# Optimization experiments

Hardware: AMD Instinct MI355X
Metric: run time of the kernel (lower is better)

Reference implementation:

```python
import jax, jax.numpy as jnp
import numpy as np

N = 4096      # nodes
E = 131072    # edges (before self loops)
C = 512       # channels
H = 8         # heads
CO = C // H   # per-head out channels (64)
EPS = 1e-5
NEG_SLOPE = 0.2


def layer_norm(x, g, b):
    mu = jnp.mean(x, axis=-1, keepdims=True)
    var = jnp.mean((x - mu) ** 2, axis=-1, keepdims=True)
    return (x - mu) * jax.lax.rsqrt(var + EPS) * g + b


def gatv2(x, src, dst, wl, bl, wr, br, att, bias):
    # PyG GATv2Conv, concat=True, add_self_loops handled by caller.
    n = x.shape[0]
    xl = (x @ wl.T + bl).reshape(n, H, CO)   # target-side features
    xr = (x @ wr.T + br).reshape(n, H, CO)   # source-side features (messages)
    e = jax.nn.leaky_relu(xl[dst] + xr[src], NEG_SLOPE)   # [E+N, H, CO]
    alpha = jnp.einsum('ehc,hc->eh', e, att)              # [E+N, H]
    # segment softmax over destination neighborhoods
    amax = jax.ops.segment_max(alpha, dst, num_segments=n)
    ex = jnp.exp(alpha - amax[dst])
    denom = jax.ops.segment_sum(ex, dst, num_segments=n)
    a = ex / denom[dst]                                   # [E+N, H]
    msg = xr[src] * a[:, :, None]                         # [E+N, H, CO]
    out = jax.ops.segment_sum(msg, dst, num_segments=n)   # [N, H, CO]
    return out.reshape(n, H * CO) + bias


def mha(x, in_w, in_b, out_w, out_b):
    # nn.MultiheadAttention self-attention, batch=1, eval mode
    n = x.shape[0]
    qkv = x @ in_w.T + in_b                               # [N, 3C]
    q, k, v = jnp.split(qkv, 3, axis=-1)
    q = q.reshape(n, H, CO); k = k.reshape(n, H, CO); v = v.reshape(n, H, CO)
    scores = jnp.einsum('qhd,khd->hqk', q, k) / jnp.sqrt(jnp.float32(CO))
    p = jax.nn.softmax(scores, axis=-1)
    o = jnp.einsum('hqk,khd->qhd', p, v).reshape(n, C)
    return o @ out_w.T + out_b


def setup_inputs() -> dict:
    key = jax.random.key(0)
    ks = jax.random.split(key, 24)
    s = 0.02
    d = {}
    d['x'] = jax.random.normal(ks[0], (N, C), jnp.float32)
    d['edge_index'] = jax.random.randint(ks[1], (2, E), 0, N, dtype=jnp.int64)
    d['gat_wl'] = jax.random.normal(ks[2], (H * CO, C), jnp.float32) * s
    d['gat_bl'] = jnp.zeros((H * CO,), jnp.float32)
    d['gat_wr'] = jax.random.normal(ks[3], (H * CO, C), jnp.float32) * s
    d['gat_br'] = jnp.zeros((H * CO,), jnp.float32)
    d['gat_att'] = jax.random.normal(ks[4], (H, CO), jnp.float32) * s
    d['gat_b'] = jnp.zeros((H * CO,), jnp.float32)
    d['in_w'] = jax.random.normal(ks[5], (3 * C, C), jnp.float32) * s
    d['in_b'] = jnp.zeros((3 * C,), jnp.float32)
    d['out_w'] = jax.random.normal(ks[6], (C, C), jnp.float32) * s
    d['out_b'] = jnp.zeros((C,), jnp.float32)
    d['ln1_g'] = jnp.ones((C,), jnp.float32); d['ln1_b'] = jnp.zeros((C,), jnp.float32)
    d['ln2_g'] = jnp.ones((C,), jnp.float32); d['ln2_b'] = jnp.zeros((C,), jnp.float32)
    d['ln3_g'] = jnp.ones((C,), jnp.float32); d['ln3_b'] = jnp.zeros((C,), jnp.float32)
    d['w1'] = jax.random.normal(ks[7], (4 * C, C), jnp.float32) * s
    d['b1'] = jnp.zeros((4 * C,), jnp.float32)
    d['w2'] = jax.random.normal(ks[8], (C, 4 * C), jnp.float32) * s
    d['b2'] = jnp.zeros((C,), jnp.float32)
    return d


def reference(x, edge_index, gat_wl, gat_bl, gat_wr, gat_br, gat_att, gat_b,
              in_w, in_b, out_w, out_b, ln1_g, ln1_b, ln2_g, ln2_b,
              ln3_g, ln3_b, w1, b1, w2, b2):
    n = x.shape[0]
    loops = jnp.arange(n, dtype=edge_index.dtype)
    src = jnp.concatenate([edge_index[0], loops])
    dst = jnp.concatenate([edge_index[1], loops])
    h_local = gatv2(x, src, dst, gat_wl, gat_bl, gat_wr, gat_br, gat_att, gat_b)
    x = layer_norm(x + h_local, ln1_g, ln1_b)
    h_global = mha(x, in_w, in_b, out_w, out_b)
    x = layer_norm(x + h_global, ln2_g, ln2_b)
    h_ffn = (jax.nn.gelu(x @ w1.T + b1, approximate=False)) @ w2.T + b2
    x = layer_norm(x + h_ffn, ln3_g, ln3_b)
    return x
```

## Files before the change

kernel.cpp:

```cpp
#include <hip/hip_runtime.h>
#include <math.h>

#define NN 4096
#define CC 512
#define EE 131072
#define NEDGE (EE + NN)
#define HH 8
#define DCO 64
#define NC2 2097152L

typedef __attribute__((ext_vector_type(8))) short bfrag;
typedef __attribute__((ext_vector_type(4))) float f32x4;
typedef __attribute__((ext_vector_type(4))) int i32x4;

__device__ __forceinline__ float bf2f(unsigned short u) {
  union { float f; unsigned int i; } x; x.i = ((unsigned int)u) << 16; return x.f;
}
__device__ __forceinline__ unsigned short f2bf(float f) {
  union { float f; unsigned int i; } x; x.f = f;
  unsigned int r = x.i + 0x7FFFu + ((x.i >> 16) & 1u);
  return (unsigned short)(r >> 16);
}
__device__ __forceinline__ unsigned short f2bf_trunc(float f) {
  union { float f; unsigned int i; } x; x.f = f;
  return (unsigned short)(x.i >> 16);
}

__device__ __forceinline__ void gld16(const unsigned short* g, unsigned short* l) {
  __builtin_amdgcn_global_load_lds(
      (__attribute__((address_space(1))) unsigned int*)g,
      (__attribute__((address_space(3))) unsigned int*)l, 16, 0, 0);
}

#define QSC 0.18033688011112042f

#define CX  2097152L
#define CWL (CX + 262144L)
#define CWR (CWL + 262144L)
#define CIW (CWR + 786432L)
#define COW (CIW + 262144L)
#define CW1 (COW + 1048576L)
#define CW2 (CW1 + 1048576L)

__global__ void cvt_all(const float* __restrict__ x, const float* __restrict__ wl,
                        const float* __restrict__ wr, const float* __restrict__ iw,
                        const float* __restrict__ ow, const float* __restrict__ w1,
                        const float* __restrict__ w2, unsigned short* __restrict__ dst,
                        int* __restrict__ cntcur, const float* __restrict__ bl,
                        const float* __restrict__ br, float* __restrict__ biasc) {
  if (blockIdx.x >= 5632) {
    int t = threadIdx.x;
    if (blockIdx.x == 5632) {
      for (int k = t; k < 8192; k += 256) cntcur[k] = 0;
    } else {
      for (int k = t; k < 512; k += 256) {
        biasc[k] = bl[k];
        biasc[512 + k] = br[k];
      }
    }
    return;
  }
  long i = ((long)blockIdx.x * 256 + threadIdx.x) * 4;
  const float* s; long o;
  if (i < CX)       { s = x;  o = i; }
  else if (i < CWL) { s = wl; o = i - CX; }
  else if (i < CWR) { s = wr; o = i - CWL; }
  else if (i < CIW) { s = iw; o = i - CWR; }
  else if (i < COW) { s = ow; o = i - CIW; }
  else if (i < CW1) { s = w1; o = i - COW; }
  else              { s = w2; o = i - CW1; }
  f32x4 v = *(const f32x4*)(s + o);
  union { unsigned long long q; unsigned short u[4]; } t;
#pragma unroll
  for (int j = 0; j < 4; j++) t.u[j] = f2bf(v[j]);
  *(unsigned long long*)(dst + i) = t.q;
}

template<int OMODE, int TN, bool SPLIT>
__global__ __launch_bounds__(256) void gemm_t(
    const unsigned short* __restrict__ A, const unsigned short* __restrict__ B,
    const float* __restrict__ bias, void* __restrict__ C,
    int K, int lda, int ldb, int ldc)
{
  __shared__ unsigned short As[4096];
  __shared__ unsigned short Bs[TN * 32];
  constexpr int MI = (TN == 128) ? 4 : 2;
  const int tid = threadIdx.x;
  const int wave = tid >> 6, lane = tid & 63;
  const int ml = lane & 15, kq = lane >> 4;
  const int wm = (TN == 128) ? ((wave >> 1) << 6) : (wave << 5);
  const int wn = (TN == 128) ? ((wave & 1) << 6) : 0;
  const int bm = blockIdx.y << 7, bn = blockIdx.x * TN;
  const int srow = tid >> 2, scol = (tid & 3) << 3;
  if (SPLIT) { A += (long)blockIdx.z * K; B += (long)blockIdx.z * K; }
  const float* biasp = (!SPLIT || blockIdx.z == 0) ? bias : nullptr;
  const unsigned short* Ag = A + (long)(bm + srow) * lda + scol;
  const unsigned short* Bg = B + (long)(bn + srow) * ldb + scol;
  const long astep = (long)64 * lda, bstep = (long)64 * ldb;
  unsigned short* lA0 = As + tid * 8;
  unsigned short* lA1 = As + 2048 + tid * 8;
  unsigned short* lB0 = Bs + tid * 8;
  f32x4 acc[MI][4];
#pragma unroll
  for (int mi = 0; mi < MI; mi++)
#pragma unroll
    for (int ni = 0; ni < 4; ni++) acc[mi][ni] = (f32x4){0.f, 0.f, 0.f, 0.f};
  for (int k0 = 0; k0 < K; k0 += 32) {
    __syncthreads();
    gld16(Ag, lA0); gld16(Ag + astep, lA1);
    gld16(Bg, lB0);
    if (TN == 128) gld16(Bg + bstep, Bs + 2048 + tid * 8);
    Ag += 32; Bg += 32;
    __syncthreads();
    bfrag af[MI], bf[4];
#pragma unroll
    for (int mi = 0; mi < MI; mi++)
      af[mi] = *(const bfrag*)&As[(wm + (mi << 4) + ml) * 32 + (kq << 3)];
#pragma unroll
    for (int ni = 0; ni < 4; ni++)
      bf[ni] = *(const bfrag*)&Bs[(wn + (ni << 4) + ml) * 32 + (kq << 3)];
#pragma unroll
    for (int mi = 0; mi < MI; mi++)
#pragma unroll
      for (int ni = 0; ni < 4; ni++)
        acc[mi][ni] = __builtin_amdgcn_mfma_f32_16x16x32_bf16(af[mi], bf[ni], acc[mi][ni], 0, 0, 0);
  }
#pragma unroll
  for (int ni = 0; ni < 4; ni++) {
    int col = bn + wn + (ni << 4) + ml;
    float bb = biasp ? biasp[col] : 0.f;
#pragma unroll
    for (int mi = 0; mi < MI; mi++) {
      int row0 = bm + wm + (mi << 4) + (kq << 2);
#pragma unroll
      for (int r = 0; r < 4; r++) {
        float v = acc[mi][ni][r] + bb;
        int row = row0 + r;
        if (OMODE == 3) {
          unsigned short* q = (unsigned short*)C;
          if (col < 512) {
            int h = col >> 6, d = col & 63;
            q[(long)h * (NN * DCO) + (long)row * DCO + d] = f2bf(v * QSC);
          } else if (col < 1024) {
            int c2 = col - 512, h = c2 >> 6, d = c2 & 63;
            q[NC2 + (long)h * (NN * DCO) + (long)row * DCO + d] = f2bf(v);
          } else {
            int c2 = col - 1024, h = c2 >> 6, d = c2 & 63;
            q[2 * NC2 + (long)h * (DCO * NN) + (long)d * NN + row] = f2bf(v);
          }
        } else if (OMODE == 0) {
          long off = (SPLIT ? (long)blockIdx.z * NC2 : 0) + (long)row * ldc + col;
          ((float*)C)[off] = v;
        } else {
          if (OMODE == 2) v = 0.5f * v * (1.f + erff(v * 0.70710678118f));
          ((unsigned short*)C)[(long)row * ldc + col] = f2bf(v);
        }
      }
    }
  }
}

__global__ void count_k(const int* __restrict__ ei, int* __restrict__ cnt) {
  int e = blockIdx.x * 256 + threadIdx.x;
  if (e >= NEDGE) return;
  int d = (e < EE) ? ei[EE + e] : (e - EE);
  atomicAdd(&cnt[d], 1);
}

__global__ void scan_k(const int* __restrict__ cnt, int* __restrict__ rowptr) {
  __shared__ int s[1024];
  int t = threadIdx.x;
  int b = t * 4;
  int c0 = cnt[b], c1 = cnt[b + 1], c2 = cnt[b + 2], c3 = cnt[b + 3];
  int sum = c0 + c1 + c2 + c3;
  s[t] = sum;
  __syncthreads();
  for (int o = 1; o < 1024; o <<= 1) {
    int v = (t >= o) ? s[t - o] : 0;
    __syncthreads();
    s[t] += v;
    __syncthreads();
  }
  int ex = s[t] - sum;
  rowptr[b] = ex; rowptr[b + 1] = ex + c0;
  rowptr[b + 2] = ex + c0 + c1; rowptr[b + 3] = ex + c0 + c1 + c2;
  if (t == 1023) rowptr[4096] = ex + sum;
}

__global__ void scatter_k(const int* __restrict__ ei, const int* __restrict__ rowptr,
                          int* __restrict__ cur, int* __restrict__ order) {
  int e = blockIdx.x * 256 + threadIdx.x;
  if (e >= NEDGE) return;
  int d = (e < EE) ? ei[EE + e] : (e - EE);
  int p = atomicAdd(&cur[d], 1);
  order[rowptr[d] + p] = e;
}

__global__ __launch_bounds__(256) void gat_fused(
    const unsigned short* __restrict__ xlr, const float* __restrict__ x,
    const int* __restrict__ order, const int* __restrict__ rowptr,
    const int* __restrict__ ei, const float* __restrict__ att,
    const float* __restrict__ gbias,
    const float* __restrict__ g, const float* __restrict__ be,
    float* __restrict__ of, unsigned short* __restrict__ ob)
{
  __shared__ float part[4][512];
  __shared__ float sw[4][8];
  __shared__ float sinv[8];
  __shared__ float shl[8];
  int n = blockIdx.x, t = threadIdx.x;
  int beg = rowptr[n], deg = rowptr[n + 1] - beg;
  int wave = t >> 6, lane = t & 63;
  int ch = lane << 3;
  union U8 { i32x4 v; unsigned short u[8]; };
  U8 XL; XL.v = *(const i32x4*)(xlr + (long)n * 1024 + ch);
  float xl[8];
#pragma unroll
  for (int j = 0; j < 8; j++) xl[j] = bf2f(XL.u[j]);
  f32x4 t0 = *(const f32x4*)(att + ch);
  f32x4 t1 = *(const f32x4*)(att + ch + 4);
  float acc[8];
#pragma unroll
  for (int j = 0; j < 8; j++) acc[j] = 0.f;
  float se = 0.f;
  int i = wave;
  U8 X;
  if (i < deg) {
    int e = order[beg + i];
    int sn = (e < EE) ? ei[e] : (e - EE);
    X.v = *(const i32x4*)(xlr + (long)sn * 1024 + 512 + ch);
  }
  while (i < deg) {
    U8 Xc = X;
    int inext = i + 4;
    if (inext < deg) {
      int e = order[beg + inext];
      int sn = (e < EE) ? ei[e] : (e - EE);
      X.v = *(const i32x4*)(xlr + (long)sn * 1024 + 512 + ch);
    }
    float xr[8];
    float p = 0.f;
#pragma unroll
    for (int j = 0; j < 8; j++) {
      xr[j] = bf2f(Xc.u[j]);
      float v = xl[j] + xr[j];
      v = (v > 0.f) ? v : 0.2f * v;
      float tv = (j < 4) ? t0[j] : t1[j - 4];
      p += tv * v;
    }
    p += __shfl_xor(p, 1); p += __shfl_xor(p, 2); p += __shfl_xor(p, 4);
    float ew = __expf(p);
    se += ew;
#pragma unroll
    for (int j = 0; j < 8; j++) acc[j] += ew * xr[j];
    i = inext;
  }
  *(f32x4*)&part[wave][ch]     = (f32x4){acc[0], acc[1], acc[2], acc[3]};
  *(f32x4*)&part[wave][ch + 4] = (f32x4){acc[4], acc[5], acc[6], acc[7]};
  if ((lane & 7) == 0) sw[wave][lane >> 3] = se;
  __syncthreads();
  if (t < 8) sinv[t] = 1.f / (sw[0][t] + sw[1][t] + sw[2][t] + sw[3][t]);
  __syncthreads();
  long base = (long)n * CC;
  float v0, v1;
  {
    int c = t;
    float p4 = part[0][c] + part[1][c] + part[2][c] + part[3][c];
    v0 = x[base + c] + p4 * sinv[c >> 6] + gbias[c];
  }
  {
    int c = t + 256;
    float p4 = part[0][c] + part[1][c] + part[2][c] + part[3][c];
    v1 = x[base + c] + p4 * sinv[c >> 6] + gbias[c];
  }
  float s = v0 + v1, ss = v0 * v0 + v1 * v1;
  for (int o = 32; o > 0; o >>= 1) { s += __shfl_down(s, o); ss += __shfl_down(ss, o); }
  if (lane == 0) { shl[wave] = s; shl[4 + wave] = ss; }
  __syncthreads();
  float S = shl[0] + shl[1] + shl[2] + shl[3];
  float SS = shl[4] + shl[5] + shl[6] + shl[7];
  float mean = S * (1.f / 512.f);
  float var = SS * (1.f / 512.f) - mean * mean;
  float rs = rsqrtf(var + 1e-5f);
  float y0 = (v0 - mean) * rs * g[t] + be[t];
  float y1 = (v1 - mean) * rs * g[t + 256] + be[t + 256];
  of[base + t] = y0; of[base + t + 256] = y1;
  ob[base + t] = f2bf(y0); ob[base + t + 256] = f2bf(y1);
}

template<int NS>
__global__ __launch_bounds__(256) void resid_ln(
    const float* __restrict__ a, const float* __restrict__ b,
    const float* __restrict__ g, const float* __restrict__ be,
    float* __restrict__ of, unsigned short* __restrict__ ob)
{
  __shared__ float sh[8];
  int row = blockIdx.x, t = threadIdx.x;
  long base = (long)row * CC;
  float b0 = 0.f, b1 = 0.f;
#pragma unroll
  for (int s = 0; s < NS; s++) {
    b0 += b[(long)s * NC2 + base + t];
    b1 += b[(long)s * NC2 + base + t + 256];
  }
  float v0 = a[base + t] + b0;
  float v1 = a[base + t + 256] + b1;
  float s = v0 + v1, ss = v0 * v0 + v1 * v1;
  for (int o = 32; o > 0; o >>= 1) { s += __shfl_down(s, o); ss += __shfl_down(ss, o); }
  int wave = t >> 6, lane = t & 63;
  if (lane == 0) { sh[wave] = s; sh[4 + wave] = ss; }
  __syncthreads();
  float S = sh[0] + sh[1] + sh[2] + sh[3];
  float SS = sh[4] + sh[5] + sh[6] + sh[7];
  float mean = S * (1.f / 512.f);
  float var = SS * (1.f / 512.f) - mean * mean;
  float rs = rsqrtf(var + 1e-5f);
  float y0 = (v0 - mean) * rs * g[t] + be[t];
  float y1 = (v1 - mean) * rs * g[t + 256] + be[t + 256];
  if (of) { of[base + t] = y0; of[base + t + 256] = y1; }
  if (ob) { ob[base + t] = f2bf(y0); ob[base + t + 256] = f2bf(y1); }
}

__global__ __launch_bounds__(256, 4) void flash_attn(
    const unsigned short* __restrict__ qkvP, unsigned short* __restrict__ Op,
    float* __restrict__ Lp)
{
  __shared__ unsigned short QP[128 * 72];
  __shared__ unsigned short Ks[64 * 72];
  __shared__ unsigned short Vs[64 * 72];
  const int tid = threadIdx.x;
  const int wave = tid >> 6, lane = tid & 63;
  const int ml = lane & 15, kq = lane >> 4;
  const int h = blockIdx.x & 7, qt = blockIdx.x >> 3;
  const int sp = blockIdx.y;
  const int n0 = qt << 7;
  const unsigned short* Qh = qkvP + (long)h * (NN * DCO);
  const unsigned short* Kh = qkvP + NC2 + (long)h * (NN * DCO);
  const unsigned short* Vh = qkvP + 2 * NC2 + (long)h * (DCO * NN);
  {
    int r = tid >> 1, c = (tid & 1) << 5;
    const unsigned short* src = Qh + (long)(n0 + r) * DCO + c;
    unsigned short* d = &QP[r * 72 + c];
    *(i32x4*)d        = *(const i32x4*)src;
    *(i32x4*)(d + 8)  = *(const i32x4*)(src + 8);
    *(i32x4*)(d + 16) = *(const i32x4*)(src + 16);
    *(i32x4*)(d + 24) = *(const i32x4*)(src + 24);
  }
  __syncthreads();
  bfrag aq[2][2];
#pragma unroll
  for (int s = 0; s < 2; s++)
#pragma unroll
    for (int kh = 0; kh < 2; kh++)
      aq[s][kh] = *(const bfrag*)&QP[(wave * 32 + s * 16 + ml) * 72 + kh * 32 + (kq << 3)];
  bfrag ones;
#pragma unroll
  for (int j = 0; j < 8; j++) ones[j] = (short)0x3F80;
  f32x4 Oa[2][4];
  f32x4 Lc[2];
#pragma unroll
  for (int s = 0; s < 2; s++) {
    Lc[s] = (f32x4){0.f, 0.f, 0.f, 0.f};
#pragma unroll
    for (int dg = 0; dg < 4; dg++) Oa[s][dg] = (f32x4){0.f, 0.f, 0.f, 0.f};
  }
  const int r_ = tid >> 2, c_ = (tid & 3) << 4;
  const int j0 = sp << 4;
  i32x4 ka, kb, va, vb;
  {
    int k0 = j0 << 6;
    ka = *(const i32x4*)(Kh + (long)(k0 + r_) * DCO + c_);
    kb = *(const i32x4*)(Kh + (long)(k0 + r_) * DCO + c_ + 8);
    va = *(const i32x4*)(Vh + (long)r_ * NN + k0 + c_);
    vb = *(const i32x4*)(Vh + (long)r_ * NN + k0 + c_ + 8);
  }
  for (int jj = 0; jj < 16; jj++) {
    if (jj) __syncthreads();
    *(i32x4*)&Ks[r_ * 72 + c_] = ka; *(i32x4*)&Ks[r_ * 72 + c_ + 8] = kb;
    *(i32x4*)&Vs[r_ * 72 + c_] = va; *(i32x4*)&Vs[r_ * 72 + c_ + 8] = vb;
    __syncthreads();
    if (jj < 15) {
      int k0 = (j0 + jj + 1) << 6;
      ka = *(const i32x4*)(Kh + (long)(k0 + r_) * DCO + c_);
      kb = *(const i32x4*)(Kh + (long)(k0 + r_) * DCO + c_ + 8);
      va = *(const i32x4*)(Vh + (long)r_ * NN + k0 + c_);
      vb = *(const i32x4*)(Vh + (long)r_ * NN + k0 + c_ + 8);
    }
    f32x4 sc[2][4];
#pragma unroll
    for (int s = 0; s < 2; s++)
#pragma unroll
      for (int c = 0; c < 4; c++) sc[s][c] = (f32x4){0.f, 0.f, 0.f, 0.f};
    __builtin_amdgcn_s_setprio(1);
#pragma unroll
    for (int c = 0; c < 4; c++) {
      bfrag bk0 = *(const bfrag*)&Ks[(c * 16 + ml) * 72 + (kq << 3)];
      bfrag bk1 = *(const bfrag*)&Ks[(c * 16 + ml) * 72 + 32 + (kq << 3)];
#pragma unroll
      for (int s = 0; s < 2; s++) {
        sc[s][c] = __builtin_amdgcn_mfma_f32_16x16x32_bf16(bk0, aq[s][0], sc[s][c], 0, 0, 0);
        sc[s][c] = __builtin_amdgcn_mfma_f32_16x16x32_bf16(bk1, aq[s][1], sc[s][c], 0, 0, 0);
      }
    }
    __builtin_amdgcn_s_setprio(0);
#pragma unroll
    for (int s = 0; s < 2; s++) {
#pragma unroll
      for (int c = 0; c < 4; c++) {
        unsigned int w0, w1;
        float e0, e1, e2, e3;
        asm("v_exp_f32 %2, %6\n\t"
            "v_exp_f32 %3, %7\n\t"
            "v_exp_f32 %4, %8\n\t"
            "v_exp_f32 %5, %9\n\t"
            "v_cvt_pk_bf16_f32 %0, %2, %3\n\t"
            "v_cvt_pk_bf16_f32 %1, %4, %5"
            : "=v"(w0), "=v"(w1), "=&v"(e0), "=&v"(e1), "=&v"(e2), "=&v"(e3)
            : "v"(sc[s][c][0]), "v"(sc[s][c][1]), "v"(sc[s][c][2]), "v"(sc[s][c][3]));
        union { unsigned long long q; unsigned int w[2]; } u;
        u.w[0] = w0; u.w[1] = w1;
        *(unsigned long long*)&QP[(wave * 32 + s * 16 + ml) * 72 + c * 16 + (kq << 2)] = u.q;
      }
    }
    bfrag ap[2][2];
#pragma unroll
    for (int s = 0; s < 2; s++)
#pragma unroll
      for (int kh = 0; kh < 2; kh++)
        ap[s][kh] = *(const bfrag*)&QP[(wave * 32 + s * 16 + ml) * 72 + kh * 32 + (kq << 3)];
    __builtin_amdgcn_s_setprio(1);
#pragma unroll
    for (int s = 0; s < 2; s++) {
      Lc[s] = __builtin_amdgcn_mfma_f32_16x16x32_bf16(ap[s][0], ones, Lc[s], 0, 0, 0);
      Lc[s] = __builtin_amdgcn_mfma_f32_16x16x32_bf16(ap[s][1], ones, Lc[s], 0, 0, 0);
    }
#pragma unroll
    for (int dg = 0; dg < 4; dg++) {
      bfrag bv0 = *(const bfrag*)&Vs[(dg * 16 + ml) * 72 + (kq << 3)];
      bfrag bv1 = *(const bfrag*)&Vs[(dg * 16 + ml) * 72 + 32 + (kq << 3)];
#pragma unroll
      for (int s = 0; s < 2; s++) {
        Oa[s][dg] = __builtin_amdgcn_mfma_f32_16x16x32_bf16(ap[s][0], bv0, Oa[s][dg], 0, 0, 0);
        Oa[s][dg] = __builtin_amdgcn_mfma_f32_16x16x32_bf16(ap[s][1], bv1, Oa[s][dg], 0, 0, 0);
      }
    }
    __builtin_amdgcn_s_setprio(0);
  }
  long obase = (long)sp * NC2;
#pragma unroll
  for (int s = 0; s < 2; s++)
#pragma unroll
    for (int dg = 0; dg < 4; dg++)
#pragma unroll
      for (int r = 0; r < 4; r++) {
        int row = wave * 32 + s * 16 + (kq << 2) + r;
        Op[obase + (long)(n0 + row) * CC + (h << 6) + (dg << 4) + ml] = f2bf(Oa[s][dg][r]);
      }
  if (ml == 0) {
#pragma unroll
    for (int s = 0; s < 2; s++)
#pragma unroll
      for (int r = 0; r < 4; r++) {
        int row = wave * 32 + s * 16 + (kq << 2) + r;
        Lp[(long)sp * (NN * HH) + (long)(n0 + row) * HH + h] = Lc[s][r];
      }
  }
}

__global__ void flash_combine(const unsigned short* __restrict__ Op,
                              const float* __restrict__ Lp,
                              unsigned short* __restrict__ Ao) {
  int idx = blockIdx.x * 256 + threadIdx.x;
  int n = idx >> 9, c = idx & 511, h = c >> 6;
  float l = 0.f, o = 0.f;
#pragma unroll
  for (int s = 0; s < 4; s++) {
    l += Lp[(long)s * (NN * HH) + (long)n * HH + h];
    o += bf2f(Op[(long)s * NC2 + idx]);
  }
  Ao[idx] = f2bf(o / l);
}

extern "C" void kernel_launch(void* const* d_in, const int* in_sizes, int n_in,
                              void* d_out, int out_size, void* d_ws, size_t ws_size,
                              hipStream_t stream) {
  typedef unsigned short u16;
  const float* x      = (const float*)d_in[0];
  const int*   ei     = (const int*)d_in[1];
  const float* wl     = (const float*)d_in[2];
  const float* bl     = (const float*)d_in[3];
  const float* wr     = (const float*)d_in[4];
  const float* br     = (const float*)d_in[5];
  const float* att    = (const float*)d_in[6];
  const float* gat_b  = (const float*)d_in[7];
  const float* in_w   = (const float*)d_in[8];
  const float* in_b   = (const float*)d_in[9];
  const float* out_w  = (const float*)d_in[10];
  const float* out_b  = (const float*)d_in[11];
  const float* ln1g   = (const float*)d_in[12];
  const float* ln1b   = (const float*)d_in[13];
  const float* ln2g   = (const float*)d_in[14];
  const float* ln2b   = (const float*)d_in[15];
  const float* ln3g   = (const float*)d_in[16];
  const float* ln3b   = (const float*)d_in[17];
  const float* w1     = (const float*)d_in[18];
  const float* b1     = (const float*)d_in[19];
  const float* w2     = (const float*)d_in[20];
  const float* b2     = (const float*)d_in[21];

  const size_t MB = 1u << 20;
  char* w = (char*)d_ws;
  float* h_f32   = (float*)(w + 0);
  float* x2_f32  = (float*)(w + 8 * MB);
  int*   cnt     = (int*)(w + 16 * MB);
  int*   cur     = cnt + 4096;
  int*   rowptr  = (int*)(w + 16 * MB + 32 * 1024);
  int*   order   = (int*)(w + 16 * MB + 64 * 1024);
  u16*   cvt     = (u16*)(w + 17 * MB);
  u16*   xbf     = cvt;
  u16*   wlrbf   = cvt + CX;
  u16*   inwbf   = cvt + CWR;
  u16*   outwbf  = cvt + CIW;
  u16*   w1bf    = cvt + COW;
  u16*   w2bf    = cvt + CW1;
  u16*   xlr_bf  = (u16*)(w + 29 * MB);
  u16*   Opart   = (u16*)(w + 29 * MB);
  float* proj    = (float*)(w + 29 * MB);
  u16*   ffn1    = (u16*)(w + 61 * MB);
  u16*   qkvP    = (u16*)(w + 93 * MB);
  float* biasc   = (float*)(w + 105 * MB);
  float* Lpart   = (float*)(w + 105 * MB);
  u16*   Ao      = (u16*)(w + 106 * MB);
  u16*   actb    = (u16*)(w + 110 * MB);

  cvt_all<<<5634, 256, 0, stream>>>(x, wl, wr, in_w, out_w, w1, w2, cvt,
                                    cnt, bl, br, biasc);
  count_k<<<(NEDGE + 255) / 256, 256, 0, stream>>>(ei, cnt);
  scan_k<<<1, 1024, 0, stream>>>(cnt, rowptr);
  scatter_k<<<(NEDGE + 255) / 256, 256, 0, stream>>>(ei, rowptr, cur, order);

  gemm_t<1, 64, false><<<dim3(16, 32), 256, 0, stream>>>(xbf, wlrbf, biasc, xlr_bf, 512, 512, 512, 1024);
  gat_fused<<<NN, 256, 0, stream>>>(xlr_bf, x, order, rowptr, ei, att, gat_b,
                                    ln1g, ln1b, h_f32, actb);

  gemm_t<3, 64, false><<<dim3(24, 32), 256, 0, stream>>>(actb, inwbf, in_b, qkvP, 512, 512, 512, 0);
  flash_attn<<<dim3(256, 4), 256, 0, stream>>>(qkvP, Opart, Lpart);
  flash_combine<<<(NN * CC) / 256, 256, 0, stream>>>(Opart, Lpart, Ao);
  gemm_t<0, 64, true><<<dim3(8, 32, 2), 256, 0, stream>>>(Ao, outwbf, out_b, proj, 256, 512, 512, 512);
  resid_ln<2><<<NN, 256, 0, stream>>>(h_f32, proj, ln2g, ln2b, x2_f32, actb);

  gemm_t<2, 128, false><<<dim3(16, 32), 256, 0, stream>>>(actb, w1bf, b1, ffn1, 512, 512, 512, 2048);
  gemm_t<0, 128, true><<<dim3(4, 32, 4), 256, 0, stream>>>(ffn1, w2bf, b2, proj, 512, 2048, 2048, 512);
  resid_ln<4><<<NN, 256, 0, stream>>>(x2_f32, proj, ln3g, ln3b, (float*)d_out, nullptr);
}
```

Measured before the change: 312.2 us.

## Double-buffer LDS tiles in GEMM and use 64-wide tiles for FFN GEMMs

```diff
diff --git a/kernel.cpp b/kernel.cpp
--- a/kernel.cpp
+++ b/kernel.cpp
@@ -82,9 +82,10 @@
     const float* __restrict__ bias, void* __restrict__ C,
     int K, int lda, int ldb, int ldc)
 {
-  __shared__ unsigned short As[4096];
-  __shared__ unsigned short Bs[TN * 32];
+  __shared__ unsigned short As[2 * 4096];
+  __shared__ unsigned short Bs[2 * TN * 32];
   constexpr int MI = (TN == 128) ? 4 : 2;
+  constexpr int BSTRIDE = TN * 32;
   const int tid = threadIdx.x;
   const int wave = tid >> 6, lane = tid & 63;
   const int ml = lane & 15, kq = lane >> 4;
@@ -97,33 +98,46 @@
   const unsigned short* Ag = A + (long)(bm + srow) * lda + scol;
   const unsigned short* Bg = B + (long)(bn + srow) * ldb + scol;
   const long astep = (long)64 * lda, bstep = (long)64 * ldb;
-  unsigned short* lA0 = As + tid * 8;
-  unsigned short* lA1 = As + 2048 + tid * 8;
-  unsigned short* lB0 = Bs + tid * 8;
   f32x4 acc[MI][4];
 #pragma unroll
   for (int mi = 0; mi < MI; mi++)
 #pragma unroll
     for (int ni = 0; ni < 4; ni++) acc[mi][ni] = (f32x4){0.f, 0.f, 0.f, 0.f};
+  gld16(Ag, As + tid * 8);
+  gld16(Ag + astep, As + 2048 + tid * 8);
+  gld16(Bg, Bs + tid * 8);
+  if (TN == 128) gld16(Bg + bstep, Bs + 2048 + tid * 8);
+  Ag += 32; Bg += 32;
+  __syncthreads();
+  int buf = 0;
   for (int k0 = 0; k0 < K; k0 += 32) {
-    __syncthreads();
-    gld16(Ag, lA0); gld16(Ag + astep, lA1);
-    gld16(Bg, lB0);
-    if (TN == 128) gld16(Bg + bstep, Bs + 2048 + tid * 8);
-    Ag += 32; Bg += 32;
-    __syncthreads();
+    const int nbuf = buf ^ 1;
+    const bool more = (k0 + 32 < K);
+    if (more) {
+      gld16(Ag, As + nbuf * 4096 + tid * 8);
+      gld16(Ag + astep, As + nbuf * 4096 + 2048 + tid * 8);
+      gld16(Bg, Bs + nbuf * BSTRIDE + tid * 8);
+      if (TN == 128) gld16(Bg + bstep, Bs + nbuf * BSTRIDE + 2048 + tid * 8);
+      Ag += 32; Bg += 32;
+    }
+    const unsigned short* Ab = As + buf * 4096;
+    const unsigned short* Bb = Bs + buf * BSTRIDE;
     bfrag af[MI], bf[4];
 #pragma unroll
     for (int mi = 0; mi < MI; mi++)
-      af[mi] = *(const bfrag*)&As[(wm + (mi << 4) + ml) * 32 + (kq << 3)];
+      af[mi] = *(const bfrag*)&Ab[(wm + (mi << 4) + ml) * 32 + (kq << 3)];
 #pragma unroll
     for (int ni = 0; ni < 4; ni++)
-      bf[ni] = *(const bfrag*)&Bs[(wn + (ni << 4) + ml) * 32 + (kq << 3)];
+      bf[ni] = *(const bfrag*)&Bb[(wn + (ni << 4) + ml) * 32 + (kq << 3)];
 #pragma unroll
     for (int mi = 0; mi < MI; mi++)
 #pragma unroll
       for (int ni = 0; ni < 4; ni++)
         acc[mi][ni] = __builtin_amdgcn_mfma_f32_16x16x32_bf16(af[mi], bf[ni], acc[mi][ni], 0, 0, 0);
+    if (more) {
+      __syncthreads();
+      buf = nbuf;
+    }
   }
 #pragma unroll
   for (int ni = 0; ni < 4; ni++) {
@@ -549,7 +563,7 @@
   gemm_t<0, 64, true><<<dim3(8, 32, 2), 256, 0, stream>>>(Ao, outwbf, out_b, proj, 256, 512, 512, 512);
   resid_ln<2><<<NN, 256, 0, stream>>>(h_f32, proj, ln2g, ln2b, x2_f32, actb);
 
-  gemm_t<2, 128, false><<<dim3(16, 32), 256, 0, stream>>>(actb, w1bf, b1, ffn1, 512, 512, 512, 2048);
-  gemm_t<0, 128, true><<<dim3(4, 32, 4), 256, 0, stream>>>(ffn1, w2bf, b2, proj, 512, 2048, 2048, 512);
+  gemm_t<2, 64, false><<<dim3(32, 32), 256, 0, stream>>>(actb, w1bf, b1, ffn1, 512, 512, 512, 2048);
+  gemm_t<0, 64, true><<<dim3(8, 32, 4), 256, 0, stream>>>(ffn1, w2bf, b2, proj, 512, 2048, 2048, 512);
   resid_ln<4><<<NN, 256, 0, stream>>>(x2_f32, proj, ln3g, ln3b, (float*)d_out, nullptr);
 }
```

Result: slower. 325.1 us (+4.1%).
